# Optimization experiments

Hardware: AMD Instinct MI355X
Metric: run time of the kernel (lower is better)

## Reference

```python
import jax, jax.numpy as jnp
import numpy as np

NUM_PROPERTIES = 10000
HDIM = 512
OUTPUT_DIM = 2
BATCH = 512
NUM_PROPS = 128


def setup_inputs() -> dict:
    key = jax.random.key(0)
    k1, k2, k3, k4 = jax.random.split(key, 4)
    hidden_states = jax.random.normal(k1, (BATCH, NUM_PROPS, HDIM), dtype=jnp.float32)
    properties = jax.random.randint(k2, (BATCH, NUM_PROPS), 0, NUM_PROPERTIES, dtype=jnp.int64)
    mask = jnp.ones((BATCH, NUM_PROPS), dtype=jnp.float32)
    # learned params: per-property classifier weight (H, D) and bias (D)
    classifier_weights = jax.random.normal(k3, (NUM_PROPERTIES, HDIM, OUTPUT_DIM), dtype=jnp.float32) * 0.02
    classifier_bias = jax.random.normal(k4, (NUM_PROPERTIES, OUTPUT_DIM), dtype=jnp.float32) * 0.02
    return {
        "hidden_states": hidden_states,
        "properties": properties,
        "mask": mask,
        "classifier_weights": classifier_weights,
        "classifier_bias": classifier_bias,
    }


def reference(hidden_states, properties, mask, classifier_weights, classifier_bias):
    # gather per-(batch, prop) weight matrices and biases
    W = classifier_weights[properties]          # (B, P, H, D)
    b = classifier_bias[properties]             # (B, P, D)
    # (B,P,1,H) @ (B,P,H,D) -> (B,P,D)
    out = jnp.einsum("bph,bphd->bpd", hidden_states, W) + b
    out = out * mask[..., None]
    return out
```

## Files before the change

kernel.cpp:

```cpp
#include <hip/hip_runtime.h>


#define H 512
#define D 2
#define CAP 48
#define KSPLIT 4
#define OVF_BLOCKS 64

__device__ __forceinline__ void gemv_one_bp(
    const float* __restrict__ hs, const float* __restrict__ mask,
    const float* __restrict__ W,  const float* __restrict__ bias,
    float* __restrict__ out, int bp, int prop, int lane)
{
    const float2* h2 = (const float2*)(hs + (size_t)bp * H);
    const float4* w4 = (const float4*)(W + (size_t)prop * (H * D));

    float2 ha = h2[lane];
    float2 hb = h2[64 + lane];
    float2 hc = h2[128 + lane];
    float2 hd = h2[192 + lane];
    float4 wa = w4[lane];
    float4 wb = w4[64 + lane];
    float4 wc = w4[128 + lane];
    float4 wd = w4[192 + lane];

    float s0 = ha.x * wa.x + ha.y * wa.z
             + hb.x * wb.x + hb.y * wb.z
             + hc.x * wc.x + hc.y * wc.z
             + hd.x * wd.x + hd.y * wd.z;
    float s1 = ha.x * wa.y + ha.y * wa.w
             + hb.x * wb.y + hb.y * wb.w
             + hc.x * wc.y + hc.y * wc.w
             + hd.x * wd.y + hd.y * wd.w;

    #pragma unroll
    for (int off = 32; off > 0; off >>= 1) {
        s0 += __shfl_xor(s0, off, 64);
        s1 += __shfl_xor(s1, off, 64);
    }

    if (lane == 0) {
        const float m  = mask[bp];
        const float b0 = bias[(size_t)prop * D + 0];
        const float b1 = bias[(size_t)prop * D + 1];
        float2 r;
        r.x = (s0 + b0) * m;
        r.y = (s1 + b1) * m;
        *(float2*)(out + (size_t)bp * D) = r;
    }
}

__global__ __launch_bounds__(256) void bucket_kernel(
    const int* __restrict__ props, int BP,
    int* __restrict__ counts,
    int* __restrict__ slots,
    int* __restrict__ ovf_cnt,
    int* __restrict__ ovf)
{
    int i = blockIdx.x * blockDim.x + threadIdx.x;
    const int stride = gridDim.x * blockDim.x;
    for (; i < BP; i += stride) {
        const int p = props[i];
        const int idx = atomicAdd(&counts[p], 1);
        if (idx < CAP) {
            slots[p * CAP + idx] = i;
        } else {
            const int o = atomicAdd(ovf_cnt, 1);
            ovf[o] = i;
        }
    }
}

__global__ __launch_bounds__(256) void per_prop_kernel(
    const float* __restrict__ hs,
    const int*   __restrict__ props,
    const float* __restrict__ mask,
    const float* __restrict__ W,
    const float* __restrict__ bias,
    float*       __restrict__ out,
    const int*   __restrict__ counts,
    const int*   __restrict__ slots,
    const int*   __restrict__ ovf_cnt,
    const int*   __restrict__ ovf,
    int nprop)
{
    const int k    = threadIdx.x >> 6;
    const int lane = threadIdx.x & 63;

    if (blockIdx.x < nprop) {
        const int p = blockIdx.x;
        int cnt = counts[p];
        if (cnt > CAP) cnt = CAP;
        if (k >= cnt) return;
        const int nt = (cnt - k + KSPLIT - 1) / KSPLIT;

        const float4* w4 = (const float4*)(W + (size_t)p * (H * D));
        const float4 wa = w4[lane];
        const float4 wb = w4[64 + lane];
        const float4 wc = w4[128 + lane];
        const float4 wd = w4[192 + lane];
        const float b0 = bias[(size_t)p * D + 0];
        const float b1 = bias[(size_t)p * D + 1];
        const float bsel = (lane & 1) ? b1 : b0;

        const int myslot = (lane < nt) ? slots[p * CAP + k + KSPLIT * lane] : 0;

        for (int u = 0; u < nt; u += 2) {
            const int  bpA  = __shfl(myslot, u, 64);
            const bool hasB = (u + 1 < nt);
            const int  bpB  = __shfl(myslot, hasB ? (u + 1) : u, 64);

            const float2* hA = (const float2*)(hs + (size_t)bpA * H);
            float2 a0 = hA[lane];
            float2 a1 = hA[64 + lane];
            float2 a2 = hA[128 + lane];
            float2 a3 = hA[192 + lane];
            float2 c0, c1, c2, c3;
            if (hasB) {
                const float2* hB = (const float2*)(hs + (size_t)bpB * H);
                c0 = hB[lane];
                c1 = hB[64 + lane];
                c2 = hB[128 + lane];
                c3 = hB[192 + lane];
            } else {
                c0 = c1 = c2 = c3 = make_float2(0.f, 0.f);
            }

            float s0A = a0.x * wa.x + a0.y * wa.z
                      + a1.x * wb.x + a1.y * wb.z
                      + a2.x * wc.x + a2.y * wc.z
                      + a3.x * wd.x + a3.y * wd.z;
            float s1A = a0.x * wa.y + a0.y * wa.w
                      + a1.x * wb.y + a1.y * wb.w
                      + a2.x * wc.y + a2.y * wc.w
                      + a3.x * wd.y + a3.y * wd.w;
            float s0B = c0.x * wa.x + c0.y * wa.z
                      + c1.x * wb.x + c1.y * wb.z
                      + c2.x * wc.x + c2.y * wc.z
                      + c3.x * wd.x + c3.y * wd.z;
            float s1B = c0.x * wa.y + c0.y * wa.w
                      + c1.x * wb.y + c1.y * wb.w
                      + c2.x * wc.y + c2.y * wc.w
                      + c3.x * wd.y + c3.y * wd.w;

            const bool o1 = (lane & 1) != 0;
            float keepA = o1 ? s1A : s0A;
            float sendA = o1 ? s0A : s1A;
            float vA = keepA + __shfl_xor(sendA, 1, 64);
            float keepB = o1 ? s1B : s0B;
            float sendB = o1 ? s0B : s1B;
            float vB = keepB + __shfl_xor(sendB, 1, 64);
            const bool o2 = (lane & 2) != 0;
            float keep = o2 ? vB : vA;
            float send = o2 ? vA : vB;
            float w = keep + __shfl_xor(send, 2, 64);
            #pragma unroll
            for (int off = 4; off <= 32; off <<= 1)
                w += __shfl_xor(w, off, 64);

            if (lane < (hasB ? 4 : 2)) {
                const int bps = (lane & 2) ? bpB : bpA;
                const float m = mask[bps];
                out[(size_t)bps * D + (lane & 1)] = (w + bsel) * m;
            }
        }
    } else {
        const int wv = (blockIdx.x - nprop) * KSPLIT + k;
        const int n = *ovf_cnt;
        for (int i = wv; i < n; i += OVF_BLOCKS * KSPLIT) {
            const int bp = ovf[i];
            gemv_one_bp(hs, mask, W, bias, out, bp, props[bp], lane);
        }
    }
}

__global__ __launch_bounds__(256) void adapter_gemv_kernel(
    const float* __restrict__ hs,
    const int*   __restrict__ props,
    const float* __restrict__ mask,
    const float* __restrict__ W,
    const float* __restrict__ bias,
    float* __restrict__ out,
    int BP)
{
    const int tid  = blockIdx.x * blockDim.x + threadIdx.x;
    const int bp   = tid >> 6;
    const int lane = tid & 63;
    if (bp >= BP) return;
    gemv_one_bp(hs, mask, W, bias, out, bp, props[bp], lane);
}

extern "C" void kernel_launch(void* const* d_in, const int* in_sizes, int n_in,
                              void* d_out, int out_size, void* d_ws, size_t ws_size,
                              hipStream_t stream) {
    const float* hs    = (const float*)d_in[0];
    const int*   props = (const int*)d_in[1];
    const float* mask  = (const float*)d_in[2];
    const float* W     = (const float*)d_in[3];
    const float* bias  = (const float*)d_in[4];
    float* out = (float*)d_out;

    const int BP    = in_sizes[1];
    const int nprop = in_sizes[3] / (H * D);

    const size_t off_counts = 0;
    const size_t off_slots  = (((size_t)nprop * 4 + 4) + 255) & ~(size_t)255;
    const size_t off_ovf    = off_slots + (size_t)nprop * CAP * 4;
    const size_t ws_needed  = off_ovf + (size_t)BP * 4;

    if (ws_size < ws_needed) {
        const int threads = 256;
        const int blocks  = (BP * 64 + threads - 1) / threads;
        adapter_gemv_kernel<<<blocks, threads, 0, stream>>>(hs, props, mask, W, bias, out, BP);
        return;
    }

    int* counts  = (int*)((char*)d_ws + off_counts);
    int* ovf_cnt = counts + nprop;
    int* slots   = (int*)((char*)d_ws + off_slots);
    int* ovf     = (int*)((char*)d_ws + off_ovf);

    hipMemsetAsync(counts, 0, off_slots, stream);

    {
        const int threads = 256;
        int blocks = (BP + threads - 1) / threads;
        if (blocks > 1024) blocks = 1024;
        bucket_kernel<<<blocks, threads, 0, stream>>>(props, BP, counts, slots, ovf_cnt, ovf);
    }

    {
        const int threads = 256;
        const int blocks  = nprop + OVF_BLOCKS;
        per_prop_kernel<<<blocks, threads, 0, stream>>>(
            hs, props, mask, W, bias, out, counts, slots, ovf_cnt, ovf, nprop);
    }
}
```

Measured before the change: 43.22 us.

## Replace memset and global-atomic bucketing with range-partitioned shared-memory bucketing

The memset launch is dropped. Each of 128 blocks now scans the whole properties array and buckets only its own property range, using shared-memory atomic counters, then writes the counts out. Overflow is split into per-block fixed-capacity lists, and CAP rises to 64 so fewer entries overflow. This removes one launch and the global atomic contention. In exchange every block reads all of props (redundant reads), and overflow beyond OVFCAP per block is silently dropped, which is a correctness risk for skewed inputs.

```diff
diff --git a/kernel.cpp b/kernel.cpp
--- a/kernel.cpp
+++ b/kernel.cpp
@@ -3,9 +3,11 @@
 
 #define H 512
 #define D 2
-#define CAP 48
+#define CAP 64
 #define KSPLIT 4
-#define OVF_BLOCKS 64
+#define NB_BUCKET 128
+#define MAX_PPB 320
+#define OVFCAP 256
 
 __device__ __forceinline__ void gemv_one_bp(
     const float* __restrict__ hs, const float* __restrict__ mask,
@@ -50,23 +52,141 @@
     }
 }
 
-__global__ __launch_bounds__(256) void bucket_kernel(
-    const int* __restrict__ props, int BP,
+__global__ __launch_bounds__(256) void bucket_zero_kernel(
+    const int* __restrict__ props, int BP, int nprop,
     int* __restrict__ counts,
     int* __restrict__ slots,
-    int* __restrict__ ovf_cnt,
-    int* __restrict__ ovf)
-{
-    int i = blockIdx.x * blockDim.x + threadIdx.x;
-    const int stride = gridDim.x * blockDim.x;
-    for (; i < BP; i += stride) {
+    int* __restrict__ ovf,
+    int* __restrict__ ovf_counts)
+{
+    __shared__ int lcnt[MAX_PPB];
+    __shared__ int lovf;
+
+    const int b   = blockIdx.x;
+    const int ppb = (nprop + NB_BUCKET - 1) / NB_BUCKET;
+    const int p0  = b * ppb;
+    const int p1  = (p0 + ppb < nprop) ? (p0 + ppb) : nprop;
+    const int np  = p1 - p0;
+    if (np <= 0) { if (threadIdx.x == 0) ovf_counts[b] = 0; return; }
+
+    for (int j = threadIdx.x; j < np; j += blockDim.x) lcnt[j] = 0;
+    if (threadIdx.x == 0) lovf = 0;
+    __syncthreads();
+
+    const int4* props4 = (const int4*)props;
+    const int n4 = BP >> 2;
+    for (int i = threadIdx.x; i < n4; i += blockDim.x) {
+        const int4 v = props4[i];
+        const int base = i << 2;
+        const int pv[4] = { v.x, v.y, v.z, v.w };
+        #pragma unroll
+        for (int c = 0; c < 4; ++c) {
+            const int p = pv[c];
+            if (p >= p0 && p < p1) {
+                const int idx = atomicAdd(&lcnt[p - p0], 1);
+                if (idx < CAP) {
+                    slots[p * CAP + idx] = base + c;
+                } else {
+                    const int o = atomicAdd(&lovf, 1);
+                    if (o < OVFCAP) ovf[b * OVFCAP + o] = base + c;
+                }
+            }
+        }
+    }
+    for (int i = (n4 << 2) + threadIdx.x; i < BP; i += blockDim.x) {
         const int p = props[i];
-        const int idx = atomicAdd(&counts[p], 1);
-        if (idx < CAP) {
-            slots[p * CAP + idx] = i;
+        if (p >= p0 && p < p1) {
+            const int idx = atomicAdd(&lcnt[p - p0], 1);
+            if (idx < CAP) {
+                slots[p * CAP + idx] = i;
+            } else {
+                const int o = atomicAdd(&lovf, 1);
+                if (o < OVFCAP) ovf[b * OVFCAP + o] = i;
+            }
+        }
+    }
+    __syncthreads();
+
+    for (int j = threadIdx.x; j < np; j += blockDim.x) counts[p0 + j] = lcnt[j];
+    if (threadIdx.x == 0) ovf_counts[b] = (lovf < OVFCAP) ? lovf : OVFCAP;
+}
+
+__device__ __forceinline__ void gemv_prop_wave(
+    const float* __restrict__ hs, const float* __restrict__ mask,
+    const float* __restrict__ W,  const float* __restrict__ bias,
+    float* __restrict__ out, const int* __restrict__ slots,
+    int p, int cnt, int k, int lane)
+{
+    const int nt = (cnt - k + KSPLIT - 1) / KSPLIT;
+    if (nt <= 0) return;
+
+    const int myslot = (lane < nt) ? slots[p * CAP + k + KSPLIT * lane] : 0;
+
+    const float4* w4 = (const float4*)(W + (size_t)p * (H * D));
+    const float4 wa = w4[lane];
+    const float4 wb = w4[64 + lane];
+    const float4 wc = w4[128 + lane];
+    const float4 wd = w4[192 + lane];
+    const float2 bv = *(const float2*)(bias + (size_t)p * D);
+    const float bsel = (lane & 1) ? bv.y : bv.x;
+
+    for (int u = 0; u < nt; u += 2) {
+        const int  bpA  = __shfl(myslot, u, 64);
+        const bool hasB = (u + 1 < nt);
+        const int  bpB  = __shfl(myslot, hasB ? (u + 1) : u, 64);
+
+        const float2* hA = (const float2*)(hs + (size_t)bpA * H);
+        float2 a0 = hA[lane];
+        float2 a1 = hA[64 + lane];
+        float2 a2 = hA[128 + lane];
+        float2 a3 = hA[192 + lane];
+        float2 c0, c1, c2, c3;
+        if (hasB) {
+            const float2* hB = (const float2*)(hs + (size_t)bpB * H);
+            c0 = hB[lane];
+            c1 = hB[64 + lane];
+            c2 = hB[128 + lane];
+            c3 = hB[192 + lane];
         } else {
-            const int o = atomicAdd(ovf_cnt, 1);
-            ovf[o] = i;
+            c0 = c1 = c2 = c3 = make_float2(0.f, 0.f);
+        }
+
+        float s0A = a0.x * wa.x + a0.y * wa.z
+                  + a1.x * wb.x + a1.y * wb.z
+                  + a2.x * wc.x + a2.y * wc.z
+                  + a3.x * wd.x + a3.y * wd.z;
+        float s1A = a0.x * wa.y + a0.y * wa.w
+                  + a1.x * wb.y + a1.y * wb.w
+                  + a2.x * wc.y + a2.y * wc.w
+                  + a3.x * wd.y + a3.y * wd.w;
+        float s0B = c0.x * wa.x + c0.y * wa.z
+                  + c1.x * wb.x + c1.y * wb.z
+                  + c2.x * wc.x + c2.y * wc.z
+                  + c3.x * wd.x + c3.y * wd.z;
+        float s1B = c0.x * wa.y + c0.y * wa.w
+                  + c1.x * wb.y + c1.y * wb.w
+                  + c2.x * wc.y + c2.y * wc.w
+                  + c3.x * wd.y + c3.y * wd.w;
+
+        const bool o1 = (lane & 1) != 0;
+        float keepA = o1 ? s1A : s0A;
+        float sendA = o1 ? s0A : s1A;
+        float vA = keepA + __shfl_xor(sendA, 1, 64);
+        float keepB = o1 ? s1B : s0B;
+        float sendB = o1 ? s0B : s1B;
+        float vB = keepB + __shfl_xor(sendB, 1, 64);
+        const bool o2 = (lane & 2) != 0;
+        float keep = o2 ? vB : vA;
+        float send = o2 ? vA : vB;
+        float w = keep + __shfl_xor(send, 2, 64);
+        #pragma unroll
+        for (int off = 4; off <= 32; off <<= 1)
+            w += __shfl_xor(w, off, 64);
+
+        if (lane < (hasB ? 4 : 2)) {
+            const int bps = (lane & 2) ? bpB : bpA;
+            const float m = mask[bps];
+            out[(size_t)bps * D + (lane & 1)] = (w + bsel) * m;
         }
     }
 }
@@ -80,95 +200,24 @@
     float*       __restrict__ out,
     const int*   __restrict__ counts,
     const int*   __restrict__ slots,
-    const int*   __restrict__ ovf_cnt,
     const int*   __restrict__ ovf,
+    const int*   __restrict__ ovf_counts,
     int nprop)
 {
     const int k    = threadIdx.x >> 6;
     const int lane = threadIdx.x & 63;
 
-    if (blockIdx.x < nprop) {
+    if (blockIdx.x < (unsigned)nprop) {
         const int p = blockIdx.x;
         int cnt = counts[p];
         if (cnt > CAP) cnt = CAP;
-        if (k >= cnt) return;
-        const int nt = (cnt - k + KSPLIT - 1) / KSPLIT;
-
-        const float4* w4 = (const float4*)(W + (size_t)p * (H * D));
-        const float4 wa = w4[lane];
-        const float4 wb = w4[64 + lane];
-        const float4 wc = w4[128 + lane];
-        const float4 wd = w4[192 + lane];
-        const float b0 = bias[(size_t)p * D + 0];
-        const float b1 = bias[(size_t)p * D + 1];
-        const float bsel = (lane & 1) ? b1 : b0;
-
-        const int myslot = (lane < nt) ? slots[p * CAP + k + KSPLIT * lane] : 0;
-
-        for (int u = 0; u < nt; u += 2) {
-            const int  bpA  = __shfl(myslot, u, 64);
-            const bool hasB = (u + 1 < nt);
-            const int  bpB  = __shfl(myslot, hasB ? (u + 1) : u, 64);
-
-            const float2* hA = (const float2*)(hs + (size_t)bpA * H);
-            float2 a0 = hA[lane];
-            float2 a1 = hA[64 + lane];
-            float2 a2 = hA[128 + lane];
-            float2 a3 = hA[192 + lane];
-            float2 c0, c1, c2, c3;
-            if (hasB) {
-                const float2* hB = (const float2*)(hs + (size_t)bpB * H);
-                c0 = hB[lane];
-                c1 = hB[64 + lane];
-                c2 = hB[128 + lane];
-                c3 = hB[192 + lane];
-            } else {
-                c0 = c1 = c2 = c3 = make_float2(0.f, 0.f);
-            }
-
-            float s0A = a0.x * wa.x + a0.y * wa.z
-                      + a1.x * wb.x + a1.y * wb.z
-                      + a2.x * wc.x + a2.y * wc.z
-                      + a3.x * wd.x + a3.y * wd.z;
-            float s1A = a0.x * wa.y + a0.y * wa.w
-                      + a1.x * wb.y + a1.y * wb.w
-                      + a2.x * wc.y + a2.y * wc.w
-                      + a3.x * wd.y + a3.y * wd.w;
-            float s0B = c0.x * wa.x + c0.y * wa.z
-                      + c1.x * wb.x + c1.y * wb.z
-                      + c2.x * wc.x + c2.y * wc.z
-                      + c3.x * wd.x + c3.y * wd.z;
-            float s1B = c0.x * wa.y + c0.y * wa.w
-                      + c1.x * wb.y + c1.y * wb.w
-                      + c2.x * wc.y + c2.y * wc.w
-                      + c3.x * wd.y + c3.y * wd.w;
-
-            const bool o1 = (lane & 1) != 0;
-            float keepA = o1 ? s1A : s0A;
-            float sendA = o1 ? s0A : s1A;
-            float vA = keepA + __shfl_xor(sendA, 1, 64);
-            float keepB = o1 ? s1B : s0B;
-            float sendB = o1 ? s0B : s1B;
-            float vB = keepB + __shfl_xor(sendB, 1, 64);
-            const bool o2 = (lane & 2) != 0;
-            float keep = o2 ? vB : vA;
-            float send = o2 ? vA : vB;
-            float w = keep + __shfl_xor(send, 2, 64);
-            #pragma unroll
-            for (int off = 4; off <= 32; off <<= 1)
-                w += __shfl_xor(w, off, 64);
-
-            if (lane < (hasB ? 4 : 2)) {
-                const int bps = (lane & 2) ? bpB : bpA;
-                const float m = mask[bps];
-                out[(size_t)bps * D + (lane & 1)] = (w + bsel) * m;
-            }
-        }
+        if (cnt == 0) return;
+        gemv_prop_wave(hs, mask, W, bias, out, slots, p, cnt, k, lane);
     } else {
-        const int wv = (blockIdx.x - nprop) * KSPLIT + k;
-        const int n = *ovf_cnt;
-        for (int i = wv; i < n; i += OVF_BLOCKS * KSPLIT) {
-            const int bp = ovf[i];
+        const int b = blockIdx.x - nprop;
+        const int n = ovf_counts[b];
+        for (int i = k; i < n; i += KSPLIT) {
+            const int bp = ovf[b * OVFCAP + i];
             gemv_one_bp(hs, mask, W, bias, out, bp, props[bp], lane);
         }
     }
@@ -204,35 +253,28 @@
     const int nprop = in_sizes[3] / (H * D);
 
     const size_t off_counts = 0;
-    const size_t off_slots  = (((size_t)nprop * 4 + 4) + 255) & ~(size_t)255;
+    const size_t off_slots  = (((size_t)nprop * 4) + 255) & ~(size_t)255;
     const size_t off_ovf    = off_slots + (size_t)nprop * CAP * 4;
-    const size_t ws_needed  = off_ovf + (size_t)BP * 4;
-
-    if (ws_size < ws_needed) {
+    const size_t off_ovfcnt = off_ovf + (size_t)NB_BUCKET * OVFCAP * 4;
+    const size_t ws_needed  = off_ovfcnt + (size_t)NB_BUCKET * 4;
+
+    const int ppb = (nprop + NB_BUCKET - 1) / NB_BUCKET;
+
+    if (ws_size < ws_needed || ppb > MAX_PPB) {
         const int threads = 256;
         const int blocks  = (BP * 64 + threads - 1) / threads;
         adapter_gemv_kernel<<<blocks, threads, 0, stream>>>(hs, props, mask, W, bias, out, BP);
         return;
     }
 
-    int* counts  = (int*)((char*)d_ws + off_counts);
-    int* ovf_cnt = counts + nprop;
-    int* slots   = (int*)((char*)d_ws + off_slots);
-    int* ovf     = (int*)((char*)d_ws + off_ovf);
-
-    hipMemsetAsync(counts, 0, off_slots, stream);
-
-    {
-        const int threads = 256;
-        int blocks = (BP + threads - 1) / threads;
-        if (blocks > 1024) blocks = 1024;
-        bucket_kernel<<<blocks, threads, 0, stream>>>(props, BP, counts, slots, ovf_cnt, ovf);
-    }
-
-    {
-        const int threads = 256;
-        const int blocks  = nprop + OVF_BLOCKS;
-        per_prop_kernel<<<blocks, threads, 0, stream>>>(
-            hs, props, mask, W, bias, out, counts, slots, ovf_cnt, ovf, nprop);
-    }
-}
+    int* counts     = (int*)((char*)d_ws + off_counts);
+    int* slots      = (int*)((char*)d_ws + off_slots);
+    int* ovf        = (int*)((char*)d_ws + off_ovf);
+    int* ovf_counts = (int*)((char*)d_ws + off_ovfcnt);
+
+    bucket_zero_kernel<<<NB_BUCKET, 256, 0, stream>>>(
+        props, BP, nprop, counts, slots, ovf, ovf_counts);
+
+    per_prop_kernel<<<nprop + NB_BUCKET, 256, 0, stream>>>(
+        hs, props, mask, W, bias, out, counts, slots, ovf, ovf_counts, nprop);
+}
```

After: 59.19 us. 37.0% more time.

## Use persistent grid-stride blocks for per-property GEMV with prefetched slot metadata

Applied to the files above, without the earlier changes.

Replaces one block per property (plus dedicated overflow blocks) with a fixed persistent grid of up to 1536 blocks that stride over properties. Each block prefetches the next property's count and slot indices while computing the current one, and the overflow work is spread across all blocks. Slot reads are limited to 12 lanes, and launch bounds request 6 blocks per CU. The aim is to cut block launch and scheduling overhead and hide metadata load latency. In exchange, load balance across properties may suffer and the slot lane cap assumes counts stay within CAP.

```diff
diff --git a/kernel.cpp b/kernel.cpp
--- a/kernel.cpp
+++ b/kernel.cpp
@@ -5,6 +5,8 @@
 #define D 2
 #define CAP 48
 #define KSPLIT 4
+#define SLOT_LANES 12
+#define GEMV_BLOCKS 1536
 #define OVF_BLOCKS 64
 
 __device__ __forceinline__ void gemv_one_bp(
@@ -71,7 +73,84 @@
     }
 }
 
-__global__ __launch_bounds__(256) void per_prop_kernel(
+__device__ __forceinline__ void gemv_prop_body(
+    const float* __restrict__ hs, const float* __restrict__ mask,
+    const float* __restrict__ W,  const float* __restrict__ bias,
+    float* __restrict__ out, int p, int cnt, int myslot, int k, int lane)
+{
+    const int nt = (cnt - k + KSPLIT - 1) / KSPLIT;
+    if (nt <= 0) return;
+
+    const float4* w4 = (const float4*)(W + (size_t)p * (H * D));
+    const float4 wa = w4[lane];
+    const float4 wb = w4[64 + lane];
+    const float4 wc = w4[128 + lane];
+    const float4 wd = w4[192 + lane];
+    const float2 bv = *(const float2*)(bias + (size_t)p * D);
+    const float bsel = (lane & 1) ? bv.y : bv.x;
+
+    for (int u = 0; u < nt; u += 2) {
+        const int  bpA  = __shfl(myslot, u, 64);
+        const bool hasB = (u + 1 < nt);
+        const int  bpB  = __shfl(myslot, hasB ? (u + 1) : u, 64);
+
+        const float2* hA = (const float2*)(hs + (size_t)bpA * H);
+        float2 a0 = hA[lane];
+        float2 a1 = hA[64 + lane];
+        float2 a2 = hA[128 + lane];
+        float2 a3 = hA[192 + lane];
+        float2 c0, c1, c2, c3;
+        if (hasB) {
+            const float2* hB = (const float2*)(hs + (size_t)bpB * H);
+            c0 = hB[lane];
+            c1 = hB[64 + lane];
+            c2 = hB[128 + lane];
+            c3 = hB[192 + lane];
+        } else {
+            c0 = c1 = c2 = c3 = make_float2(0.f, 0.f);
+        }
+
+        float s0A = a0.x * wa.x + a0.y * wa.z
+                  + a1.x * wb.x + a1.y * wb.z
+                  + a2.x * wc.x + a2.y * wc.z
+                  + a3.x * wd.x + a3.y * wd.z;
+        float s1A = a0.x * wa.y + a0.y * wa.w
+                  + a1.x * wb.y + a1.y * wb.w
+                  + a2.x * wc.y + a2.y * wc.w
+                  + a3.x * wd.y + a3.y * wd.w;
+        float s0B = c0.x * wa.x + c0.y * wa.z
+                  + c1.x * wb.x + c1.y * wb.z
+                  + c2.x * wc.x + c2.y * wc.z
+                  + c3.x * wd.x + c3.y * wd.z;
+        float s1B = c0.x * wa.y + c0.y * wa.w
+                  + c1.x * wb.y + c1.y * wb.w
+                  + c2.x * wc.y + c2.y * wc.w
+                  + c3.x * wd.y + c3.y * wd.w;
+
+        const bool o1 = (lane & 1) != 0;
+        float keepA = o1 ? s1A : s0A;
+        float sendA = o1 ? s0A : s1A;
+        float vA = keepA + __shfl_xor(sendA, 1, 64);
+        float keepB = o1 ? s1B : s0B;
+        float sendB = o1 ? s0B : s1B;
+        float vB = keepB + __shfl_xor(sendB, 1, 64);
+        const bool o2 = (lane & 2) != 0;
+        float keep = o2 ? vB : vA;
+        float send = o2 ? vA : vB;
+        float w = keep + __shfl_xor(send, 2, 64);
+        #pragma unroll
+        for (int off = 4; off <= 32; off <<= 1)
+            w += __shfl_xor(w, off, 64);
+
+        if (lane < (hasB ? 4 : 2)) {
+            const int bps = (lane & 2) ? bpB : bpA;
+            const float m = mask[bps];
+            out[(size_t)bps * D + (lane & 1)] = (w + bsel) * m;
+        }
+    }
+}
+
+__global__ __launch_bounds__(256, 6) void per_prop_kernel(
     const float* __restrict__ hs,
     const int*   __restrict__ props,
     const float* __restrict__ mask,
@@ -86,88 +165,39 @@
 {
     const int k    = threadIdx.x >> 6;
     const int lane = threadIdx.x & 63;
-
-    if (blockIdx.x < nprop) {
-        const int p = blockIdx.x;
-        int cnt = counts[p];
-        if (cnt > CAP) cnt = CAP;
-        if (k >= cnt) return;
-        const int nt = (cnt - k + KSPLIT - 1) / KSPLIT;
-
-        const float4* w4 = (const float4*)(W + (size_t)p * (H * D));
-        const float4 wa = w4[lane];
-        const float4 wb = w4[64 + lane];
-        const float4 wc = w4[128 + lane];
-        const float4 wd = w4[192 + lane];
-        const float b0 = bias[(size_t)p * D + 0];
-        const float b1 = bias[(size_t)p * D + 1];
-        const float bsel = (lane & 1) ? b1 : b0;
-
-        const int myslot = (lane < nt) ? slots[p * CAP + k + KSPLIT * lane] : 0;
-
-        for (int u = 0; u < nt; u += 2) {
-            const int  bpA  = __shfl(myslot, u, 64);
-            const bool hasB = (u + 1 < nt);
-            const int  bpB  = __shfl(myslot, hasB ? (u + 1) : u, 64);
-
-            const float2* hA = (const float2*)(hs + (size_t)bpA * H);
-            float2 a0 = hA[lane];
-            float2 a1 = hA[64 + lane];
-            float2 a2 = hA[128 + lane];
-            float2 a3 = hA[192 + lane];
-            float2 c0, c1, c2, c3;
-            if (hasB) {
-                const float2* hB = (const float2*)(hs + (size_t)bpB * H);
-                c0 = hB[lane];
-                c1 = hB[64 + lane];
-                c2 = hB[128 + lane];
-                c3 = hB[192 + lane];
-            } else {
-                c0 = c1 = c2 = c3 = make_float2(0.f, 0.f);
-            }
-
-            float s0A = a0.x * wa.x + a0.y * wa.z
-                      + a1.x * wb.x + a1.y * wb.z
-                      + a2.x * wc.x + a2.y * wc.z
-                      + a3.x * wd.x + a3.y * wd.z;
-            float s1A = a0.x * wa.y + a0.y * wa.w
-                      + a1.x * wb.y + a1.y * wb.w
-                      + a2.x * wc.y + a2.y * wc.w
-                      + a3.x * wd.y + a3.y * wd.w;
-            float s0B = c0.x * wa.x + c0.y * wa.z
-                      + c1.x * wb.x + c1.y * wb.z
-                      + c2.x * wc.x + c2.y * wc.z
-                      + c3.x * wd.x + c3.y * wd.z;
-            float s1B = c0.x * wa.y + c0.y * wa.w
-                      + c1.x * wb.y + c1.y * wb.w
-                      + c2.x * wc.y + c2.y * wc.w
-                      + c3.x * wd.y + c3.y * wd.w;
-
-            const bool o1 = (lane & 1) != 0;
-            float keepA = o1 ? s1A : s0A;
-            float sendA = o1 ? s0A : s1A;
-            float vA = keepA + __shfl_xor(sendA, 1, 64);
-            float keepB = o1 ? s1B : s0B;
-            float sendB = o1 ? s0B : s1B;
-            float vB = keepB + __shfl_xor(sendB, 1, 64);
-            const bool o2 = (lane & 2) != 0;
-            float keep = o2 ? vB : vA;
-            float send = o2 ? vA : vB;
-            float w = keep + __shfl_xor(send, 2, 64);
-            #pragma unroll
-            for (int off = 4; off <= 32; off <<= 1)
-                w += __shfl_xor(w, off, 64);
-
-            if (lane < (hasB ? 4 : 2)) {
-                const int bps = (lane & 2) ? bpB : bpA;
-                const float m = mask[bps];
-                out[(size_t)bps * D + (lane & 1)] = (w + bsel) * m;
-            }
-        }
-    } else {
-        const int wv = (blockIdx.x - nprop) * KSPLIT + k;
-        const int n = *ovf_cnt;
-        for (int i = wv; i < n; i += OVF_BLOCKS * KSPLIT) {
+    const int G    = gridDim.x;
+
+    int p = blockIdx.x;
+    int cnt_cur  = 0;
+    int slot_cur = 0;
+    if (p < nprop) {
+        cnt_cur = counts[p];
+        if (lane < SLOT_LANES)
+            slot_cur = slots[p * CAP + k + KSPLIT * lane];
+    }
+
+    for (; p < nprop; p += G) {
+        const int pn = p + G;
+        int cnt_next = 0, slot_next = 0;
+        if (pn < nprop) {
+            cnt_next = counts[pn];
+            if (lane < SLOT_LANES)
+                slot_next = slots[pn * CAP + k + KSPLIT * lane];
+        }
+
+        int cnt = (cnt_cur > CAP) ? CAP : cnt_cur;
+        if (cnt > 0)
+            gemv_prop_body(hs, mask, W, bias, out, p, cnt, slot_cur, k, lane);
+
+        cnt_cur  = cnt_next;
+        slot_cur = slot_next;
+    }
+
+    const int nov = *ovf_cnt;
+    if (nov > 0) {
+        const int gwid = blockIdx.x * KSPLIT + k;
+        const int totw = G * KSPLIT;
+        for (int i = gwid; i < nov; i += totw) {
             const int bp = ovf[i];
             gemv_one_bp(hs, mask, W, bias, out, bp, props[bp], lane);
         }
@@ -231,7 +261,8 @@
 
     {
         const int threads = 256;
-        const int blocks  = nprop + OVF_BLOCKS;
+        int blocks = GEMV_BLOCKS;
+        if (blocks > nprop) blocks = nprop;
         per_prop_kernel<<<blocks, threads, 0, stream>>>(
             hs, props, mask, W, bias, out, counts, slots, ovf_cnt, ovf, nprop);
     }
```

Result: slower. 45.23 us (+4.7%).
